# Kernel optimization log

Measured on AMD Instinct MI355X. Metric: run time of the kernel, lower is better.

Reference implementation:

```python
import jax, jax.numpy as jnp
import numpy as np

N, E, DIN, HID, H, ED = 50000, 800000, 128, 64, 4, 5
Z_IDX = 3          # impedance column
PHYS_W = 1.0       # physics_weight
NEG_SLOPE = 0.2    # GATv2 leaky_relu slope


def gat_layer(x, src, dst, ea, Wl, bl, Wr, br, We, att, temp, bias, concat):
    """PhysicsGATv2Conv (add_self_loops=False, eval mode / no dropout)."""
    n = x.shape[0]
    Hh, C = att.shape
    xl = (x @ Wl + bl).reshape(n, Hh, C)   # lin_l -> source features
    xr = (x @ Wr + br).reshape(n, Hh, C)   # lin_r -> target features
    # physics-enhanced edge attr: overwrite last column with temp * w / |Z|
    z = jnp.clip(ea[:, Z_IDX], 1e-6, None)
    ea = ea.at[:, -1].set(temp * PHYS_W / z)
    e = (ea @ We).reshape(-1, Hh, C)       # lin_edge (no bias)
    m = jax.nn.leaky_relu(xl[src] + xr[dst] + e, NEG_SLOPE)  # [E,H,C]
    logit = jnp.einsum('ehc,hc->eh', m, att)                 # [E,H]
    # segment softmax over incoming edges of each target node
    lmax = jax.ops.segment_max(logit, dst, num_segments=n)
    w = jnp.exp(logit - lmax[dst])
    den = jax.ops.segment_sum(w, dst, num_segments=n)
    a = w / (den[dst] + 1e-16)
    out = jax.ops.segment_sum(xl[src] * a[:, :, None], dst, num_segments=n)
    out = out.reshape(n, Hh * C) if concat else out.mean(axis=1)
    return out + bias


def layer_norm(x, w, b):
    mu = x.mean(-1, keepdims=True)
    v = ((x - mu) ** 2).mean(-1, keepdims=True)
    return (x - mu) * jax.lax.rsqrt(v + 1e-5) * w + b


def setup_inputs() -> dict:
    key = jax.random.key(0)
    ks = iter(jax.random.split(key, 40))
    nk = lambda: next(ks)
    d = {}
    d['x'] = jax.random.normal(nk(), (N, DIN), jnp.float32)
    d['edge_index'] = jax.random.randint(nk(), (2, E), 0, N)
    d['edge_attr'] = jax.random.uniform(nk(), (E, ED), jnp.float32)
    hd = HID * H
    cfg = [(DIN, True), (hd, True), (hd, False)]
    for i, (din, concat) in enumerate(cfg):
        dout = hd if concat else HID
        d[f'Wl{i}'] = jax.random.normal(nk(), (din, hd), jnp.float32) / np.sqrt(din)
        d[f'bl{i}'] = 0.01 * jax.random.normal(nk(), (hd,), jnp.float32)
        d[f'Wr{i}'] = jax.random.normal(nk(), (din, hd), jnp.float32) / np.sqrt(din)
        d[f'br{i}'] = 0.01 * jax.random.normal(nk(), (hd,), jnp.float32)
        d[f'We{i}'] = jax.random.normal(nk(), (ED, hd), jnp.float32) / np.sqrt(ED)
        d[f'att{i}'] = jax.random.normal(nk(), (H, HID), jnp.float32) / np.sqrt(HID)
        d[f'temp{i}'] = jnp.float32(1.0)
        d[f'bias{i}'] = 0.01 * jax.random.normal(nk(), (dout,), jnp.float32)
        d[f'lnw{i}'] = jnp.ones((dout,), jnp.float32)
        d[f'lnb{i}'] = jnp.zeros((dout,), jnp.float32)
    d['pw0'] = jax.random.normal(nk(), (DIN, hd), jnp.float32) / np.sqrt(DIN)
    d['pb0'] = jnp.zeros((hd,), jnp.float32)
    d['pw2'] = jax.random.normal(nk(), (hd, HID), jnp.float32) / np.sqrt(hd)
    d['pb2'] = jnp.zeros((HID,), jnp.float32)
    return d


def reference(x, edge_index, edge_attr,
              Wl0, bl0, Wr0, br0, We0, att0, temp0, bias0, lnw0, lnb0,
              Wl1, bl1, Wr1, br1, We1, att1, temp1, bias1, lnw1, lnb1,
              Wl2, bl2, Wr2, br2, We2, att2, temp2, bias2, lnw2, lnb2,
              pw0, pb0, pw2, pb2):
    src, dst = edge_index[0], edge_index[1]
    # layer 0: 128 -> 256 (concat), residual projected
    h = gat_layer(x, src, dst, edge_attr, Wl0, bl0, Wr0, br0, We0, att0, temp0, bias0, True)
    h = layer_norm(h, lnw0, lnb0) + (x @ pw0 + pb0)
    h = jax.nn.elu(h)
    # layer 1: 256 -> 256 (concat), identity residual
    h1 = gat_layer(h, src, dst, edge_attr, Wl1, bl1, Wr1, br1, We1, att1, temp1, bias1, True)
    h = layer_norm(h1, lnw1, lnb1) + h
    h = jax.nn.elu(h)
    # layer 2: 256 -> 64 (head-mean), residual projected, no activation
    h2 = gat_layer(h, src, dst, edge_attr, Wl2, bl2, Wr2, br2, We2, att2, temp2, bias2, False)
    out = layer_norm(h2, lnw2, lnb2) + (h @ pw2 + pb2)
    return out
```

## Files before the change

### kernel.cpp

```cpp
#include <hip/hip_runtime.h>
#include <math.h>

#define NN 50000
#define EE 800000
#define NB 196

typedef _Float16 half8 __attribute__((ext_vector_type(8)));
typedef _Float16 hv4  __attribute__((ext_vector_type(4)));
typedef _Float16 hv2  __attribute__((ext_vector_type(2)));
typedef float floatx16 __attribute__((ext_vector_type(16)));
typedef float fv4 __attribute__((ext_vector_type(4)));

__device__ __forceinline__ float fexp2(float x) { return __builtin_amdgcn_exp2f(x); }

template<int CTRL>
__device__ __forceinline__ float dppadd(float x) {
    int t = __builtin_amdgcn_update_dpp(0, __float_as_int(x), CTRL, 0xf, 0xf, false);
    return x + __int_as_float(t);
}
__device__ __forceinline__ float red16(float x) {
    x = dppadd<0x121>(x);
    x = dppadd<0x122>(x);
    x = dppadd<0x124>(x);
    x = dppadd<0x128>(x);
    return x;
}

__global__ __launch_bounds__(256) void swizzleA(
    const float* __restrict__ A, _Float16* __restrict__ Asw, int M, int K)
{
    int wave = threadIdx.x >> 6, lane = threadIdx.x & 63;
    int tile = blockIdx.x;
    int kc = blockIdx.y * 4 + wave;
    int KC = K >> 4;
    int row = tile * 32 + (lane & 31);
    int k0 = kc * 16 + (lane >> 5) * 8;
    float4 v0 = make_float4(0.f, 0.f, 0.f, 0.f);
    float4 v1 = make_float4(0.f, 0.f, 0.f, 0.f);
    if (row < M) {
        const float* p = A + (size_t)row * K + k0;
        v0 = *(const float4*)p;
        v1 = *(const float4*)(p + 4);
    }
    half8 o;
    o[0] = (_Float16)v0.x; o[1] = (_Float16)v0.y;
    o[2] = (_Float16)v0.z; o[3] = (_Float16)v0.w;
    o[4] = (_Float16)v1.x; o[5] = (_Float16)v1.y;
    o[6] = (_Float16)v1.z; o[7] = (_Float16)v1.w;
    *(half8*)(Asw + (((size_t)tile * KC + kc) * 64 + lane) * 8) = o;
}

__global__ __launch_bounds__(256) void prep_weights(
    const float* __restrict__ s0, const float* __restrict__ s1,
    const float* __restrict__ s2, const float* __restrict__ s3,
    const float* __restrict__ s4, const float* __restrict__ s5,
    const float* __restrict__ s6, const float* __restrict__ s7,
    _Float16* __restrict__ catB0, _Float16* __restrict__ catB1,
    _Float16* __restrict__ catB2,
    const float* __restrict__ bl0, const float* __restrict__ br0,
    const float* __restrict__ pb0, const float* __restrict__ bl1,
    const float* __restrict__ br1, const float* __restrict__ bl2,
    const float* __restrict__ br2, const float* __restrict__ pb2,
    float* __restrict__ cb0, float* __restrict__ cb1, float* __restrict__ cb2)
{
    int b = blockIdx.x;
    if (b >= 184) {
        int t = (b - 184) * 256 + threadIdx.x;
        if (t < 768) {
            cb0[t] = (t < 256) ? bl0[t] : (t < 512) ? br0[t - 256] : pb0[t - 512];
        } else if (t < 1280) {
            int u = t - 768;
            cb1[u] = (u < 256) ? bl1[u] : br1[u - 256];
        } else if (t < 1856) {
            int u = t - 1280;
            cb2[u] = (u < 256) ? bl2[u] : (u < 512) ? br2[u - 256] : pb2[u - 512];
        }
        return;
    }
    int wave = threadIdx.x >> 6, lane = threadIdx.x & 63;
    int pair = b * 4 + wave;
    const int cum[9] = {0, 64, 128, 192, 320, 448, 576, 704, 736};
    int job = 0;
    while (pair >= cum[job + 1]) ++job;
    const float* srcs[8] = {s0, s1, s2, s3, s4, s5, s6, s7};
    const int KCs[8] = {8, 8, 8, 16, 16, 16, 16, 16};
    const int NCs[8] = {256, 256, 256, 256, 256, 256, 256, 64};
    const int ntb[8] = {0, 8, 16, 0, 8, 0, 8, 16};
    _Float16* dsts[8] = {catB0, catB0, catB0, catB1, catB1, catB2, catB2, catB2};
    int p = pair - cum[job];
    int KC = KCs[job], NC = NCs[job];
    int nt = p / KC, kc = p - nt * KC;
    int n = (nt >> 1) * 64 + ((lane & 31) * 2) + (nt & 1);
    int k0 = kc * 16 + (lane >> 5) * 8;
    const float* B = srcs[job];
    half8 o;
#pragma unroll
    for (int jj = 0; jj < 8; ++jj)
        o[jj] = (_Float16)B[(size_t)(k0 + jj) * NC + n];
    int ntG = ntb[job] + nt;
    *(half8*)(dsts[job] + (((size_t)ntG * KC + kc) * 64 + lane) * 8) = o;
}

__global__ __launch_bounds__(256) void gemm_mfma(
    const _Float16* __restrict__ Asw, const _Float16* __restrict__ Bsw,
    const float* __restrict__ bias, _Float16* __restrict__ C,
    int M, int K, int NC)
{
    const int wave = threadIdx.x >> 6, lane = threadIdx.x & 63;
    const int KC = K >> 4;
    const int rt0 = blockIdx.x * 4 + (wave & 1) * 2;
    const int NG = NC >> 6;
    int g = blockIdx.y * 2 + (wave >> 1);
    if (g >= NG) g = NG - 1;

    const half8* Ap0 = (const half8*)Asw + (size_t)rt0 * KC * 64 + lane;
    const half8* Ap1 = Ap0 + (size_t)KC * 64;
    const half8* Bp0 = (const half8*)Bsw + (size_t)(2 * g) * KC * 64 + lane;
    const half8* Bp1 = Bp0 + (size_t)KC * 64;

    floatx16 accE0 = {0.f}, accE1 = {0.f}, accO0 = {0.f}, accO1 = {0.f};

#pragma unroll 4
    for (int kc = 0; kc < KC; ++kc) {
        half8 a0 = Ap0[(size_t)kc * 64];
        half8 a1 = Ap1[(size_t)kc * 64];
        half8 b0 = Bp0[(size_t)kc * 64];
        half8 b1 = Bp1[(size_t)kc * 64];
        accE0 = __builtin_amdgcn_mfma_f32_32x32x16_f16(a0, b0, accE0, 0, 0, 0);
        accE1 = __builtin_amdgcn_mfma_f32_32x32x16_f16(a1, b0, accE1, 0, 0, 0);
        accO0 = __builtin_amdgcn_mfma_f32_32x32x16_f16(a0, b1, accO0, 0, 0, 0);
        accO1 = __builtin_amdgcn_mfma_f32_32x32x16_f16(a1, b1, accO1, 0, 0, 0);
    }

    const int nlane = lane & 31, hs = lane >> 5;
    int colb = g * 64 + nlane * 2;
    float be = bias[colb], bo = bias[colb + 1];
#pragma unroll
    for (int r = 0; r < 16; ++r) {
        int rowin = (r & 3) + 8 * (r >> 2) + 4 * hs;
        int row0 = rt0 * 32 + rowin;
        int row1 = row0 + 32;
        if (row0 < M) {
            hv2 pe;
            pe[0] = (_Float16)(accE0[r] + be);
            pe[1] = (_Float16)(accO0[r] + bo);
            *(hv2*)(C + (size_t)row0 * NC + colb) = pe;
        }
        if (row1 < M) {
            hv2 po;
            po[0] = (_Float16)(accE1[r] + be);
            po[1] = (_Float16)(accO1[r] + bo);
            *(hv2*)(C + (size_t)row1 * NC + colb) = po;
        }
    }
}

__global__ __launch_bounds__(256) void hist_kernel(const int* __restrict__ dst,
                                                   int* __restrict__ deg)
{
    int e = blockIdx.x * 256 + threadIdx.x;
    if (e < EE) atomicAdd(&deg[dst[e]], 1);
}

__global__ __launch_bounds__(256) void scan_local(const int* __restrict__ deg,
                                                  int* __restrict__ rowoff,
                                                  int* __restrict__ part)
{
    __shared__ int sd[256];
    int tid = threadIdx.x;
    int i = blockIdx.x * 256 + tid;
    int v = (i < NN) ? deg[i] : 0;
    sd[tid] = v;
    __syncthreads();
    for (int off = 1; off < 256; off <<= 1) {
        int t = (tid >= off) ? sd[tid - off] : 0;
        __syncthreads();
        sd[tid] += t;
        __syncthreads();
    }
    if (i < NN) rowoff[i] = sd[tid] - v;
    if (tid == 255) part[blockIdx.x] = sd[255];
}

__global__ __launch_bounds__(256) void scan_part(int* __restrict__ part,
                                                 int* __restrict__ rowoff)
{
    __shared__ int sd[256];
    int tid = threadIdx.x;
    int v = (tid < NB) ? part[tid] : 0;
    sd[tid] = v;
    __syncthreads();
    for (int off = 1; off < 256; off <<= 1) {
        int t = (tid >= off) ? sd[tid - off] : 0;
        __syncthreads();
        sd[tid] += t;
        __syncthreads();
    }
    if (tid < NB) part[tid] = sd[tid] - v;
    if (tid == 0) rowoff[NN] = EE;
}

__global__ __launch_bounds__(256) void scan_add(int* __restrict__ rowoff,
                                                const int* __restrict__ part,
                                                int* __restrict__ cursor)
{
    int i = blockIdx.x * 256 + threadIdx.x;
    if (i < NN) {
        rowoff[i] += part[blockIdx.x];
        cursor[i] = 0;
    }
}

__global__ __launch_bounds__(256) void scatter_kernel(
    const int* __restrict__ src, const int* __restrict__ dst,
    const float* __restrict__ ea, const int* __restrict__ rowoff,
    int* __restrict__ cursor, int* __restrict__ srcp,
    float4* __restrict__ eap, float* __restrict__ erec)
{
    int e = blockIdx.x * 256 + threadIdx.x;
    if (e < EE) {
        int d = dst[e];
        int pos = rowoff[d] + atomicAdd(&cursor[d], 1);
        srcp[pos] = src[e];
        const float* p = ea + (size_t)e * 5;
        eap[pos] = make_float4(p[0], p[1], p[2], p[3]);
        erec[pos] = 1.0f / fmaxf(p[3], 1e-6f);
    }
}

__global__ __launch_bounds__(256) void fused_attn_ln(
    const int* __restrict__ rowoff, const int* __restrict__ srcp,
    const float4* __restrict__ eap, const float* __restrict__ erec,
    const _Float16* __restrict__ xlp, int rstride,
    const float* __restrict__ We, const float* __restrict__ att,
    const float* __restrict__ temp, const float* __restrict__ bias,
    const float* __restrict__ lnw, const float* __restrict__ lnb,
    const _Float16* __restrict__ residH, const float* __restrict__ residF,
    float* __restrict__ outF, _Float16* __restrict__ aswOut, int mode)
{
    int v = __builtin_amdgcn_readfirstlane(blockIdx.x * 4 + (threadIdx.x >> 6));
    int lane = threadIdx.x & 63;
    if (v >= NN) return;
    int grp = lane >> 4;
    int sub = lane & 15;
    int j = grp * 64 + sub * 4;

    fv4 ww0 = *(const fv4*)(We + j);
    fv4 ww1 = *(const fv4*)(We + 256 + j);
    fv4 ww2 = *(const fv4*)(We + 512 + j);
    fv4 ww3 = *(const fv4*)(We + 768 + j);
    fv4 ww4 = *(const fv4*)(We + 1024 + j);
    fv4 atv = *(const fv4*)(att + j);
    fv4 xrv = __builtin_convertvector(
        *(const hv4*)(xlp + (size_t)v * rstride + 256 + j), fv4);
    float tmp = temp[0];
    const float L2E = 1.44269504088896340736f;

    float mxd = -INFINITY, dend = 0.f;
    fv4 acc = {0.f, 0.f, 0.f, 0.f};

    int beg = rowoff[v], end = rowoff[v + 1];
    int i = beg;
    for (; i + 4 <= end; i += 4) {
        int s[4]; float4 a[4]; float q[4]; fv4 xv[4]; float l[4];
#pragma unroll
        for (int u = 0; u < 4; ++u) {
            s[u] = srcp[i + u];
            a[u] = eap[i + u];
            q[u] = tmp * erec[i + u];
        }
#pragma unroll
        for (int u = 0; u < 4; ++u)
            xv[u] = __builtin_convertvector(
                *(const hv4*)(xlp + (size_t)s[u] * rstride + j), fv4);
#pragma unroll
        for (int u = 0; u < 4; ++u) {
            fv4 m = xv[u] + xrv;
            m = m + a[u].x * ww0; m = m + a[u].y * ww1; m = m + a[u].z * ww2;
            m = m + a[u].w * ww3; m = m + q[u] * ww4;
            m = __builtin_elementwise_max(m, m * 0.2f);
            fv4 p = m * atv;
            l[u] = (p[0] + p[1]) + (p[2] + p[3]);
        }
#pragma unroll
        for (int u = 0; u < 4; ++u) l[u] = red16(l[u]) * L2E;
        float nm = fmaxf(fmaxf(l[0], l[1]), fmaxf(l[2], l[3]));
        nm = fmaxf(nm, mxd);
        float sc = fexp2(mxd - nm);
        float e0 = fexp2(l[0] - nm);
        float e1 = fexp2(l[1] - nm);
        float e2 = fexp2(l[2] - nm);
        float e3 = fexp2(l[3] - nm);
        mxd = nm;
        dend = dend * sc + ((e0 + e1) + (e2 + e3));
        acc = acc * sc +
              ((xv[0] * e0 + xv[1] * e1) + (xv[2] * e2 + xv[3] * e3));
    }
    for (; i < end; ++i) {
        int s0 = srcp[i];
        float4 a0 = eap[i];
        float q0 = tmp * erec[i];
        fv4 x0 = __builtin_convertvector(
            *(const hv4*)(xlp + (size_t)s0 * rstride + j), fv4);
        fv4 m0 = x0 + xrv;
        m0 = m0 + a0.x * ww0; m0 = m0 + a0.y * ww1; m0 = m0 + a0.z * ww2;
        m0 = m0 + a0.w * ww3; m0 = m0 + q0 * ww4;
        m0 = __builtin_elementwise_max(m0, m0 * 0.2f);
        fv4 p0 = m0 * atv;
        float l0 = (p0[0] + p0[1]) + (p0[2] + p0[3]);
        l0 = red16(l0) * L2E;
        float nm = fmaxf(mxd, l0);
        float sc = fexp2(mxd - nm);
        float e0 = fexp2(l0 - nm);
        mxd = nm;
        dend = dend * sc + e0;
        acc = acc * sc + x0 * e0;
    }

    float inv = __builtin_amdgcn_rcpf(dend + 1e-16f);
    if (mode <= 1) {
        fv4 bb = *(const fv4*)(bias + j);
        fv4 o = acc * inv + bb;
        float s  = (o[0] + o[1]) + (o[2] + o[3]);
        fv4 oq = o * o;
        float s2 = (oq[0] + oq[1]) + (oq[2] + oq[3]);
        s = red16(s);   s += __shfl_xor(s, 16, 64);  s += __shfl_xor(s, 32, 64);
        s2 = red16(s2); s2 += __shfl_xor(s2, 16, 64); s2 += __shfl_xor(s2, 32, 64);
        float mu = s * (1.f / 256.f);
        float var = s2 * (1.f / 256.f) - mu * mu;
        float rs = __builtin_amdgcn_rsqf(var + 1e-5f);
        fv4 lw = *(const fv4*)(lnw + j);
        fv4 lb = *(const fv4*)(lnb + j);
        fv4 rr;
        if (mode == 0)
            rr = __builtin_convertvector(
                *(const hv4*)(residH + (size_t)v * rstride + j), fv4);
        else
            rr = *(const fv4*)(residF + (size_t)v * 256 + j);
        fv4 y = (o - mu) * rs * lw + lb + rr;
        y[0] = (y[0] > 0.f) ? y[0] : fexp2(y[0] * L2E) - 1.f;
        y[1] = (y[1] > 0.f) ? y[1] : fexp2(y[1] * L2E) - 1.f;
        y[2] = (y[2] > 0.f) ? y[2] : fexp2(y[2] * L2E) - 1.f;
        y[3] = (y[3] > 0.f) ? y[3] : fexp2(y[3] * L2E) - 1.f;
        if (mode == 0)
            *(fv4*)(outF + (size_t)v * 256 + j) = y;
        int kc = j >> 4, half = (j >> 3) & 1, off = j & 7;
        size_t idx = (((size_t)(v >> 5) * 16 + kc) * 64 + (v & 31) + 32 * half) * 8 + off;
        hv4 yh = __builtin_convertvector(y, hv4);
        *(hv4*)(aswOut + idx) = yh;
    } else {
        fv4 r = acc * inv;
        r[0] += __shfl_xor(r[0], 16, 64); r[0] += __shfl_xor(r[0], 32, 64);
        r[1] += __shfl_xor(r[1], 16, 64); r[1] += __shfl_xor(r[1], 32, 64);
        r[2] += __shfl_xor(r[2], 16, 64); r[2] += __shfl_xor(r[2], 32, 64);
        r[3] += __shfl_xor(r[3], 16, 64); r[3] += __shfl_xor(r[3], 32, 64);
        fv4 bb = *(const fv4*)(bias + sub * 4);
        fv4 o = r * 0.25f + bb;
        float s  = (o[0] + o[1]) + (o[2] + o[3]);
        fv4 oq = o * o;
        float s2 = (oq[0] + oq[1]) + (oq[2] + oq[3]);
        s = red16(s);
        s2 = red16(s2);
        float mu = s * (1.f / 64.f);
        float var = s2 * (1.f / 64.f) - mu * mu;
        float rs = __builtin_amdgcn_rsqf(var + 1e-5f);
        fv4 lw = *(const fv4*)(lnw + sub * 4);
        fv4 lb = *(const fv4*)(lnb + sub * 4);
        fv4 rr = __builtin_convertvector(
            *(const hv4*)(residH + (size_t)v * rstride + sub * 4), fv4);
        fv4 y = (o - mu) * rs * lw + lb + rr;
        if (grp == 0)
            *(fv4*)(outF + (size_t)v * 64 + sub * 4) = y;
    }
}

extern "C" void kernel_launch(void* const* d_in, const int* in_sizes, int n_in,
                              void* d_out, int out_size, void* d_ws, size_t ws_size,
                              hipStream_t stream)
{
    const float* x    = (const float*)d_in[0];
    const int*   eidx = (const int*)d_in[1];
    const float* ea   = (const float*)d_in[2];
    const int* src = eidx;
    const int* dst = eidx + EE;

    const float *Wl[3], *bl[3], *Wr[3], *br[3], *We[3], *att[3], *temp[3],
                *bias[3], *lnw[3], *lnb[3];
    for (int i = 0; i < 3; ++i) {
        int b = 3 + i * 10;
        Wl[i]   = (const float*)d_in[b + 0];
        bl[i]   = (const float*)d_in[b + 1];
        Wr[i]   = (const float*)d_in[b + 2];
        br[i]   = (const float*)d_in[b + 3];
        We[i]   = (const float*)d_in[b + 4];
        att[i]  = (const float*)d_in[b + 5];
        temp[i] = (const float*)d_in[b + 6];
        bias[i] = (const float*)d_in[b + 7];
        lnw[i]  = (const float*)d_in[b + 8];
        lnb[i]  = (const float*)d_in[b + 9];
    }
    const float* pw0 = (const float*)d_in[33];
    const float* pb0 = (const float*)d_in[34];
    const float* pw2 = (const float*)d_in[35];
    const float* pb2 = (const float*)d_in[36];

    char* w = (char*)d_ws;
    float* h     = (float*)w; w += (size_t)NN * 256 * 4;
    char*  gbase = w;         w += (size_t)NN * 256 * 4;
    _Float16* xlr = (_Float16*)w; w += (size_t)NN * 768 * 2;
    float4* eap  = (float4*)w; w += (size_t)EE * 16;
    float* erec  = (float*)w; w += (size_t)EE * 4;
    int* srcp    = (int*)w;   w += (size_t)EE * 4;
    int* rowoff  = (int*)w;   w += (size_t)(NN + 16) * 4;
    int* cursor  = (int*)w;   w += (size_t)NN * 4;
    int* part    = (int*)w;   w += 1024;
    w = (char*)(((uintptr_t)w + 255) & ~(uintptr_t)255);
    _Float16* catB0 = (_Float16*)w; w += 196608;
    _Float16* catB1 = (_Float16*)w; w += 262144;
    _Float16* catB2 = (_Float16*)w; w += 294912;
    float* cb0 = (float*)w; w += 768 * 4;
    float* cb1 = (float*)w; w += 512 * 4;
    float* cb2 = (float*)w; w += 576 * 4;
    _Float16* Asw = (_Float16*)gbase;

    dim3 blk(256);
    dim3 grid_e((EE + 255) / 256);
    dim3 grid_nw((NN + 3) / 4);
    dim3 grid_nb(NB);
    const int MT = 391;

    auto attn = [&](int L, int rstride, const _Float16* residH,
                    const float* residF, float* outFp, _Float16* asw, int mode) {
        fused_attn_ln<<<grid_nw, blk, 0, stream>>>(
            rowoff, srcp, eap, erec, xlr, rstride, We[L], att[L], temp[L],
            bias[L], lnw[L], lnb[L], residH, residF, outFp, asw, mode);
    };

    hipMemsetAsync(cursor, 0, (size_t)NN * 4, stream);
    hipLaunchKernelGGL(hist_kernel, grid_e, blk, 0, stream, dst, cursor);
    hipLaunchKernelGGL(scan_local, grid_nb, blk, 0, stream, cursor, rowoff, part);
    hipLaunchKernelGGL(scan_part, dim3(1), blk, 0, stream, part, rowoff);
    hipLaunchKernelGGL(scan_add, grid_nb, blk, 0, stream, rowoff, part, cursor);
    hipLaunchKernelGGL(scatter_kernel, grid_e, blk, 0, stream,
                       src, dst, ea, rowoff, cursor, srcp, eap, erec);

    hipLaunchKernelGGL(prep_weights, dim3(192), blk, 0, stream,
                       Wl[0], Wr[0], pw0, Wl[1], Wr[1], Wl[2], Wr[2], pw2,
                       catB0, catB1, catB2,
                       bl[0], br[0], pb0, bl[1], br[1], bl[2], br[2], pb2,
                       cb0, cb1, cb2);

    swizzleA<<<dim3(4 * MT, 2), blk, 0, stream>>>(x, Asw, NN, 128);
    gemm_mfma<<<dim3(MT, 6), blk, 0, stream>>>(
        Asw, catB0, cb0, xlr, NN, 128, 768);
    attn(0, 768, xlr + 512, nullptr, h, Asw, 0);

    gemm_mfma<<<dim3(MT, 4), blk, 0, stream>>>(
        Asw, catB1, cb1, xlr, NN, 256, 512);
    attn(1, 512, nullptr, h, nullptr, Asw, 1);

    gemm_mfma<<<dim3(MT, 5), blk, 0, stream>>>(
        Asw, catB2, cb2, xlr, NN, 256, 576);
    attn(2, 576, xlr + 512, nullptr, (float*)d_out, nullptr, 2);
}
```

Before: 656.3 us.

## Stage GEMM B tiles in LDS and template attention kernel on mode/stride

The MFMA GEMM now loads each block's 64-column B panel into shared memory once and lets four waves each cover two row tiles against it. Before, every wave read B from global memory. The grid changes to 196 row blocks by one column group per block. The attention/LayerNorm kernel is templated on mode and row stride so branches and index arithmetic resolve at compile time. The B staging adds a barrier and 32KB of LDS per block, which can lower occupancy. swizzleA gains a bounds guard because its grid is now larger.

```diff
diff --git a/kernel.cpp b/kernel.cpp
--- a/kernel.cpp
+++ b/kernel.cpp
@@ -33,6 +33,7 @@
     int tile = blockIdx.x;
     int kc = blockIdx.y * 4 + wave;
     int KC = K >> 4;
+    if (kc >= KC) return;
     int row = tile * 32 + (lane & 31);
     int k0 = kc * 16 + (lane >> 5) * 8;
     float4 v0 = make_float4(0.f, 0.f, 0.f, 0.f);
@@ -106,17 +107,24 @@
     const float* __restrict__ bias, _Float16* __restrict__ C,
     int M, int K, int NC)
 {
+    __shared__ _Float16 lb[16384];
     const int wave = threadIdx.x >> 6, lane = threadIdx.x & 63;
     const int KC = K >> 4;
-    const int rt0 = blockIdx.x * 4 + (wave & 1) * 2;
-    const int NG = NC >> 6;
-    int g = blockIdx.y * 2 + (wave >> 1);
-    if (g >= NG) g = NG - 1;
-
+    const int g = blockIdx.y;
+
+    {
+        const _Float16* srcB = Bsw + (size_t)(2 * g) * KC * 512;
+        int total = 2 * KC * 512;
+        for (int t = threadIdx.x * 8; t < total; t += 2048)
+            *(half8*)(lb + t) = *(const half8*)(srcB + t);
+    }
+    __syncthreads();
+
+    const int rt0 = blockIdx.x * 8 + wave * 2;
     const half8* Ap0 = (const half8*)Asw + (size_t)rt0 * KC * 64 + lane;
     const half8* Ap1 = Ap0 + (size_t)KC * 64;
-    const half8* Bp0 = (const half8*)Bsw + (size_t)(2 * g) * KC * 64 + lane;
-    const half8* Bp1 = Bp0 + (size_t)KC * 64;
+    const half8* Bl0 = (const half8*)lb + lane;
+    const half8* Bl1 = (const half8*)lb + (size_t)KC * 64 + lane;
 
     floatx16 accE0 = {0.f}, accE1 = {0.f}, accO0 = {0.f}, accO1 = {0.f};
 
@@ -124,8 +132,8 @@
     for (int kc = 0; kc < KC; ++kc) {
         half8 a0 = Ap0[(size_t)kc * 64];
         half8 a1 = Ap1[(size_t)kc * 64];
-        half8 b0 = Bp0[(size_t)kc * 64];
-        half8 b1 = Bp1[(size_t)kc * 64];
+        half8 b0 = Bl0[(size_t)kc * 64];
+        half8 b1 = Bl1[(size_t)kc * 64];
         accE0 = __builtin_amdgcn_mfma_f32_32x32x16_f16(a0, b0, accE0, 0, 0, 0);
         accE1 = __builtin_amdgcn_mfma_f32_32x32x16_f16(a1, b0, accE1, 0, 0, 0);
         accO0 = __builtin_amdgcn_mfma_f32_32x32x16_f16(a0, b1, accO0, 0, 0, 0);
@@ -228,15 +236,16 @@
     }
 }
 
+template<int MODE, int RSTRIDE>
 __global__ __launch_bounds__(256) void fused_attn_ln(
     const int* __restrict__ rowoff, const int* __restrict__ srcp,
     const float4* __restrict__ eap, const float* __restrict__ erec,
-    const _Float16* __restrict__ xlp, int rstride,
+    const _Float16* __restrict__ xlp,
     const float* __restrict__ We, const float* __restrict__ att,
     const float* __restrict__ temp, const float* __restrict__ bias,
     const float* __restrict__ lnw, const float* __restrict__ lnb,
     const _Float16* __restrict__ residH, const float* __restrict__ residF,
-    float* __restrict__ outF, _Float16* __restrict__ aswOut, int mode)
+    float* __restrict__ outF, _Float16* __restrict__ aswOut)
 {
     int v = __builtin_amdgcn_readfirstlane(blockIdx.x * 4 + (threadIdx.x >> 6));
     int lane = threadIdx.x & 63;
@@ -252,7 +261,7 @@
     fv4 ww4 = *(const fv4*)(We + 1024 + j);
     fv4 atv = *(const fv4*)(att + j);
     fv4 xrv = __builtin_convertvector(
-        *(const hv4*)(xlp + (size_t)v * rstride + 256 + j), fv4);
+        *(const hv4*)(xlp + (size_t)v * RSTRIDE + 256 + j), fv4);
     float tmp = temp[0];
     const float L2E = 1.44269504088896340736f;
 
@@ -272,7 +281,7 @@
 #pragma unroll
         for (int u = 0; u < 4; ++u)
             xv[u] = __builtin_convertvector(
-                *(const hv4*)(xlp + (size_t)s[u] * rstride + j), fv4);
+                *(const hv4*)(xlp + (size_t)s[u] * RSTRIDE + j), fv4);
 #pragma unroll
         for (int u = 0; u < 4; ++u) {
             fv4 m = xv[u] + xrv;
@@ -301,7 +310,7 @@
         float4 a0 = eap[i];
         float q0 = tmp * erec[i];
         fv4 x0 = __builtin_convertvector(
-            *(const hv4*)(xlp + (size_t)s0 * rstride + j), fv4);
+            *(const hv4*)(xlp + (size_t)s0 * RSTRIDE + j), fv4);
         fv4 m0 = x0 + xrv;
         m0 = m0 + a0.x * ww0; m0 = m0 + a0.y * ww1; m0 = m0 + a0.z * ww2;
         m0 = m0 + a0.w * ww3; m0 = m0 + q0 * ww4;
@@ -318,7 +327,7 @@
     }
 
     float inv = __builtin_amdgcn_rcpf(dend + 1e-16f);
-    if (mode <= 1) {
+    if (MODE <= 1) {
         fv4 bb = *(const fv4*)(bias + j);
         fv4 o = acc * inv + bb;
         float s  = (o[0] + o[1]) + (o[2] + o[3]);
@@ -332,9 +341,9 @@
         fv4 lw = *(const fv4*)(lnw + j);
         fv4 lb = *(const fv4*)(lnb + j);
         fv4 rr;
-        if (mode == 0)
+        if (MODE == 0)
             rr = __builtin_convertvector(
-                *(const hv4*)(residH + (size_t)v * rstride + j), fv4);
+                *(const hv4*)(residH + (size_t)v * RSTRIDE + j), fv4);
         else
             rr = *(const fv4*)(residF + (size_t)v * 256 + j);
         fv4 y = (o - mu) * rs * lw + lb + rr;
@@ -342,7 +351,7 @@
         y[1] = (y[1] > 0.f) ? y[1] : fexp2(y[1] * L2E) - 1.f;
         y[2] = (y[2] > 0.f) ? y[2] : fexp2(y[2] * L2E) - 1.f;
         y[3] = (y[3] > 0.f) ? y[3] : fexp2(y[3] * L2E) - 1.f;
-        if (mode == 0)
+        if (MODE == 0)
             *(fv4*)(outF + (size_t)v * 256 + j) = y;
         int kc = j >> 4, half = (j >> 3) & 1, off = j & 7;
         size_t idx = (((size_t)(v >> 5) * 16 + kc) * 64 + (v & 31) + 32 * half) * 8 + off;
@@ -367,7 +376,7 @@
         fv4 lw = *(const fv4*)(lnw + sub * 4);
         fv4 lb = *(const fv4*)(lnb + sub * 4);
         fv4 rr = __builtin_convertvector(
-            *(const hv4*)(residH + (size_t)v * rstride + sub * 4), fv4);
+            *(const hv4*)(residH + (size_t)v * RSTRIDE + sub * 4), fv4);
         fv4 y = (o - mu) * rs * lw + lb + rr;
         if (grp == 0)
             *(fv4*)(outF + (size_t)v * 64 + sub * 4) = y;
@@ -427,14 +436,7 @@
     dim3 grid_e((EE + 255) / 256);
     dim3 grid_nw((NN + 3) / 4);
     dim3 grid_nb(NB);
-    const int MT = 391;
-
-    auto attn = [&](int L, int rstride, const _Float16* residH,
-                    const float* residF, float* outFp, _Float16* asw, int mode) {
-        fused_attn_ln<<<grid_nw, blk, 0, stream>>>(
-            rowoff, srcp, eap, erec, xlr, rstride, We[L], att[L], temp[L],
-            bias[L], lnw[L], lnb[L], residH, residF, outFp, asw, mode);
-    };
+    const int RB = 196;
 
     hipMemsetAsync(cursor, 0, (size_t)NN * 4, stream);
     hipLaunchKernelGGL(hist_kernel, grid_e, blk, 0, stream, dst, cursor);
@@ -450,16 +452,22 @@
                        bl[0], br[0], pb0, bl[1], br[1], bl[2], br[2], pb2,
                        cb0, cb1, cb2);
 
-    swizzleA<<<dim3(4 * MT, 2), blk, 0, stream>>>(x, Asw, NN, 128);
-    gemm_mfma<<<dim3(MT, 6), blk, 0, stream>>>(
+    swizzleA<<<dim3(1568, 2), blk, 0, stream>>>(x, Asw, NN, 128);
+    gemm_mfma<<<dim3(RB, 12), blk, 0, stream>>>(
         Asw, catB0, cb0, xlr, NN, 128, 768);
-    attn(0, 768, xlr + 512, nullptr, h, Asw, 0);
-
-    gemm_mfma<<<dim3(MT, 4), blk, 0, stream>>>(
+    fused_attn_ln<0, 768><<<grid_nw, blk, 0, stream>>>(
+        rowoff, srcp, eap, erec, xlr, We[0], att[0], temp[0],
+        bias[0], lnw[0], lnb[0], xlr + 512, nullptr, h, Asw);
+
+    gemm_mfma<<<dim3(RB, 8), blk, 0, stream>>>(
         Asw, catB1, cb1, xlr, NN, 256, 512);
-    attn(1, 512, nullptr, h, nullptr, Asw, 1);
-
-    gemm_mfma<<<dim3(MT, 5), blk, 0, stream>>>(
+    fused_attn_ln<1, 512><<<grid_nw, blk, 0, stream>>>(
+        rowoff, srcp, eap, erec, xlr, We[1], att[1], temp[1],
+        bias[1], lnw[1], lnb[1], nullptr, h, nullptr, Asw);
+
+    gemm_mfma<<<dim3(RB, 9), blk, 0, stream>>>(
         Asw, catB2, cb2, xlr, NN, 256, 576);
-    attn(2, 576, xlr + 512, nullptr, (float*)d_out, nullptr, 2);
-}
+    fused_attn_ln<2, 576><<<grid_nw, blk, 0, stream>>>(
+        rowoff, srcp, eap, erec, xlr, We[2], att[2], temp[2],
+        bias[2], lnw[2], lnb[2], xlr + 512, nullptr, (float*)d_out, nullptr);
+}
```

Measured after the change: 676.9 us. +3.1%, slower.
